# Performance work log

Hardware: AMD Instinct MI355X
Metric: run time of the kernel (lower is better)

The kernel has to match this reference:

```python
import jax, jax.numpy as jnp
import numpy as np

NJ, ND, NQ, NC, NAV = 4, 32, 32, 64, 2
N = 131072

def silu(x):
    return x * jax.nn.sigmoid(x)

def conv1d(x, w, b, stride=1):
    # x: [n, Cin, L], w: [Cout, Cin, K] (torch OIH layout)
    y = jax.lax.conv_general_dilated(x, w, (stride,), 'VALID',
                                     dimension_numbers=('NCH', 'OIH', 'NCH'))
    return y + b[None, :, None]

def dijet_cat(x, d):
    # x: [n, nd, 12], d: [n, nd, 6] -> interleave pairs of x with d -> [n, nd, 18]
    n, nd, _ = x.shape
    return jnp.concatenate([x.reshape(n, nd, 6, 2), d[..., None]], axis=3).reshape(n, nd, 18)

def quad_cat(x, q):
    # x: [n, nq, 6], q: [n, nq, 3] -> [n, nq, 9]
    n, nq, _ = x.shape
    return jnp.concatenate([x.reshape(n, nq, 3, 2), q[..., None]], axis=3).reshape(n, nq, 9)

def rotate(p, R):
    return p.at[:, 2, :].set(((p[:, 2, :] + 1.0 + R) % 2.0) - 1.0)

def flip_phi(p):
    return p.at[:, 2, :].multiply(-1.0)

def flip_eta(p):
    return p.at[:, 1, :].multiply(-1.0)

def inv_part(p, da, qa, W_td, b_td, W_db, b_db, W_dr1, b_dr1, W_dr2, b_dr2,
             W_tq, b_tq, W_qb, b_qb, W_qr1, b_qr1, W_qr2, b_qr2):
    p = conv1d(p, W_td, b_td)                 # [n, nd, 12]
    d = conv1d(p, W_db, b_db, stride=2)       # [n, nd-2, 6]
    d = jnp.concatenate([d, da], axis=1)      # [n, nd, 6]
    d0 = d
    d = silu(d)
    d = conv1d(dijet_cat(p, d), W_dr1, b_dr1, stride=3) + d0
    d = silu(d)
    d = conv1d(dijet_cat(p, d), W_dr2, b_dr2, stride=3) + d0
    d = silu(d)
    d = conv1d(d, W_tq, b_tq)                 # [n, nq, 6]
    q = conv1d(d, W_qb, b_qb, stride=2)       # [n, nq-2, 3]
    q = jnp.concatenate([q, qa], axis=1)      # [n, nq, 3]
    q0 = q
    q = silu(q)
    q = conv1d(quad_cat(d, q), W_qr1, b_qr1, stride=3) + q0
    q = silu(q)
    q = conv1d(quad_cat(d, q), W_qr2, b_qr2, stride=3) + q0
    return silu(q)                            # [n, nq, 3]

def setup_inputs() -> dict:
    key = jax.random.key(0)
    ks = jax.random.split(key, 24)
    s = 0.1
    inp = {
        'x': jax.random.normal(ks[0], (N, NJ, 12), jnp.float32),
        'p': jax.random.normal(ks[1], (N, NJ, 12), jnp.float32),
        'da': jax.random.normal(ks[2], (N, 12), jnp.float32),
        'qa': jax.random.normal(ks[3], (N, 6), jnp.float32),
        'va': jax.random.normal(ks[4], (N, NAV), jnp.float32),
        'W_td': jax.random.normal(ks[5], (ND, NJ, 1), jnp.float32) * s,
        'b_td': jax.random.normal(ks[6], (ND,), jnp.float32) * s,
        'W_db': jax.random.normal(ks[7], (ND - 2, ND, 2), jnp.float32) * s,
        'b_db': jax.random.normal(ks[8], (ND - 2,), jnp.float32) * s,
        'W_dr1': jax.random.normal(ks[9], (ND, ND, 3), jnp.float32) * s,
        'b_dr1': jax.random.normal(ks[10], (ND,), jnp.float32) * s,
        'W_dr2': jax.random.normal(ks[11], (ND, ND, 3), jnp.float32) * s,
        'b_dr2': jax.random.normal(ks[12], (ND,), jnp.float32) * s,
        'W_tq': jax.random.normal(ks[13], (NQ, ND, 1), jnp.float32) * s,
        'b_tq': jax.random.normal(ks[14], (NQ,), jnp.float32) * s,
        'W_qb': jax.random.normal(ks[15], (NQ - 2, NQ, 2), jnp.float32) * s,
        'b_qb': jax.random.normal(ks[16], (NQ - 2,), jnp.float32) * s,
        'W_qr1': jax.random.normal(ks[17], (NQ, NQ, 3), jnp.float32) * s,
        'b_qr1': jax.random.normal(ks[18], (NQ,), jnp.float32) * s,
        'W_qr2': jax.random.normal(ks[19], (NQ, NQ, 3), jnp.float32) * s,
        'b_qr2': jax.random.normal(ks[20], (NQ,), jnp.float32) * s,
        'W_tv': jax.random.normal(ks[21], (NC, NQ + NAV, 1), jnp.float32) * s,
        'b_tv': jax.random.normal(ks[22], (NC,), jnp.float32) * s,
        'W_v1': jax.random.normal(jax.random.fold_in(key, 101), (NC, NC, 1), jnp.float32) * s,
        'b_v1': jax.random.normal(jax.random.fold_in(key, 102), (NC,), jnp.float32) * s,
        'W_v2': jax.random.normal(jax.random.fold_in(key, 103), (NC, NC, 1), jnp.float32) * s,
        'b_v2': jax.random.normal(jax.random.fold_in(key, 104), (NC,), jnp.float32) * s,
        'W_vs': jax.random.normal(jax.random.fold_in(key, 105), (1, NC, 3), jnp.float32) * s,
        'b_vs': jax.random.normal(jax.random.fold_in(key, 106), (1,), jnp.float32) * s,
    }
    return inp

def reference(x, p, da, qa, va,
              W_td, b_td, W_db, b_db, W_dr1, b_dr1, W_dr2, b_dr2,
              W_tq, b_tq, W_qb, b_qb, W_qr1, b_qr1, W_qr2, b_qr2,
              W_tv, b_tv, W_v1, b_v1, W_v2, b_v2, W_vs, b_vs):
    n = p.shape[0]
    da2 = da.reshape(n, 2, 6)
    qa2 = qa.reshape(n, 2, 3)
    va3 = jnp.broadcast_to(va[:, :NAV, None], (n, NAV, 3))
    params = (W_td, b_td, W_db, b_db, W_dr1, b_dr1, W_dr2, b_dr2,
              W_tq, b_tq, W_qb, b_qb, W_qr1, b_qr1, W_qr2, b_qr2)
    # eval mode: nR=1, R=[0], randomR=0; 4-fold phi/eta flip symmetrization
    p0 = rotate(p, 0.0)
    p1 = flip_phi(p0)
    p2 = flip_eta(p1)
    p3 = flip_eta(p0)
    q = (inv_part(p0, da2, qa2, *params) + inv_part(p1, da2, qa2, *params)
         + inv_part(p2, da2, qa2, *params) + inv_part(p3, da2, qa2, *params)) / 4.0
    v = jnp.concatenate([q, va3], axis=1)     # [n, nq+nAv, 3]
    v = conv1d(v, W_tv, b_tv)                 # [n, nc, 3]
    v0 = v
    v = silu(v)
    v = conv1d(v, W_v1, b_v1) + v0
    v = silu(v)
    v = conv1d(v, W_v2, b_v2) + v0
    v = silu(v)
    v = conv1d(v, W_vs, b_vs)                 # [n, 1, 1]
    return v.reshape(n, -1)
```

## Files before the change

### kernel.cpp

```cpp
#include <hip/hip_runtime.h>


typedef _Float16 f16x8 __attribute__((ext_vector_type(8)));
typedef float f32x4 __attribute__((ext_vector_type(4)));
typedef __fp16 fp16x2 __attribute__((ext_vector_type(2)));

#define TILES 50
#define WS_BIAS    12800
#define NBIAS      416
#define QSUM_DW    13216

__device__ __forceinline__ float silu_f(float x){
    return x * __builtin_amdgcn_rcpf(1.0f + __expf(-x));
}
__device__ __forceinline__ f32x4 silu4(f32x4 v){
    f32x4 r; r.x=silu_f(v.x); r.y=silu_f(v.y); r.z=silu_f(v.z); r.w=silu_f(v.w);
    return r;
}
__device__ __forceinline__ unsigned pk(float a, float b){
    fp16x2 h = __builtin_amdgcn_cvt_pkrtz(a, b);
    return __builtin_bit_cast(unsigned, h);
}


__device__ float l1_Ad0(const float* Wdb, const float* Wtd, int c, int k){
    int h = k>>2, jr = k&3; float a = 0.f;
    for (int i=0;i<32;++i) a += Wdb[64*c+2*i+h]*Wtd[4*i+jr];
    return a;
}
__device__ float l1_AB(const float* Wdb,const float* bdb,const float* btd,int c){
    float b = bdb[c];
    for (int i=0;i<32;++i) b += (Wdb[64*c+2*i]+Wdb[64*c+2*i+1])*btd[i];
    return b;
}
__device__ float l1_M(const float* Wdr,const float* Wtd,int c,int k){
    int h=k>>2, jr=k&3; float a=0.f;
    for(int i=0;i<32;++i) a += Wdr[96*c+3*i+h]*Wtd[4*i+jr];
    return a;
}
__device__ float l1_MB(const float* Wdr,const float* bdr,const float* btd,int c){
    float b = bdr[c];
    for(int i=0;i<32;++i) b += (Wdr[96*c+3*i]+Wdr[96*c+3*i+1])*btd[i];
    return b;
}
__device__ float qn_Q(const float* Wqb, const float* Wtq, int c, int kg){
    int z=kg>>5, kk=kg&31; float a=0.f;
    for(int i=0;i<32;++i) a += Wqb[64*c+2*i+z]*Wtq[32*i+kk];
    return a;
}
__device__ float qn_N(const float* Wqr, const float* Wtq, int c, int kg){
    int z=kg>>5, kk=kg&31; float a=0.f;
    for(int i=0;i<32;++i) a += Wqr[96*c+3*i+z]*Wtq[32*i+kk];
    return a;
}

__global__ void precompute(
    const float* __restrict__ Wtd, const float* __restrict__ btd,
    const float* __restrict__ Wdb, const float* __restrict__ bdb,
    const float* __restrict__ Wdr1, const float* __restrict__ bdr1,
    const float* __restrict__ Wdr2, const float* __restrict__ bdr2,
    const float* __restrict__ Wtq, const float* __restrict__ btq,
    const float* __restrict__ Wqb, const float* __restrict__ bqb,
    const float* __restrict__ Wqr1, const float* __restrict__ bqr1,
    const float* __restrict__ Wqr2, const float* __restrict__ bqr2,
    const float* __restrict__ Wtv, const float* __restrict__ btv,
    const float* __restrict__ Wv1, const float* __restrict__ bv1,
    const float* __restrict__ Wv2, const float* __restrict__ bv2,
    const float* __restrict__ Wvs,
    float* __restrict__ wsf)
{
    const int tid = blockIdx.x*blockDim.x + threadIdx.x;
    const int stride = gridDim.x*blockDim.x;

    for (int it = tid; it < TILES*64; it += stride) {
        const int tile = it >> 6, lane = it & 63;
        const int m = lane & 15, g = lane >> 4;
        float v[8];
        #pragma unroll
        for (int j = 0; j < 8; ++j) {
            const int k = 8*g + j;
            float val = 0.f;
            if (tile < 6) {
                const int r = 16*tile + m;
                if (r < 32) {
                    if (r < 30) {
                        if (k < 8)      val = l1_Ad0(Wdb, Wtd, r, k);
                        else if (k==8)  val = l1_AB(Wdb, bdb, btd, r);
                    } else if (r == 30) val = (k==9)  ? 1.f : 0.f;
                    else                val = (k==10) ? 1.f : 0.f;
                } else {
                    const float* Wdr = (r<64)? Wdr1 : Wdr2;
                    const float* bdr = (r<64)? bdr1 : bdr2;
                    const int c = (r<64)? r-32 : r-64;
                    if (k < 8) {
                        val = l1_M(Wdr, Wtd, c, k);
                        if (c < 30) val += l1_Ad0(Wdb, Wtd, c, k);
                    } else if (k == 8) {
                        val = l1_MB(Wdr, bdr, btd, c);
                        if (c < 30) val += l1_AB(Wdb, bdb, btd, c);
                    } else if (k == 9)  val = (c==30)? 1.f : 0.f;
                    else if (k == 10)   val = (c==31)? 1.f : 0.f;
                }
            } else if (tile < 8)  { val = Wdr1[96*(16*(tile-6)+m) + 3*k + 2]; }
            else if (tile < 10)   { val = Wdr2[96*(16*(tile-8)+m) + 3*k + 2]; }
            else if (tile < 22) {
                const int tt = tile-10, r = 16*(tt>>1)+m, kg = 32*(tt&1)+k;
                if (r < 32) { if (r < 30) val = qn_Q(Wqb, Wtq, r, kg); }
                else {
                    const float* Wqr = (r<64)? Wqr1 : Wqr2;
                    const int c = (r<64)? r-32 : r-64;
                    val = qn_N(Wqr, Wtq, c, kg);
                    if (c < 30) val += qn_Q(Wqb, Wtq, c, kg);
                }
            }
            else if (tile < 24)  { val = Wqr1[96*(16*(tile-22)+m) + 3*k + 2]; }
            else if (tile < 26)  { val = Wqr2[96*(16*(tile-24)+m) + 3*k + 2]; }
            else if (tile < 34) {
                const int tt = tile-26, r = 16*(tt>>1)+m;
                if ((tt&1)==0) val = 0.25f*Wtv[34*r + k];
                else {
                    if (k==0) val = btv[r];
                    else if (k==1) val = Wtv[34*r+32];
                    else if (k==2) val = Wtv[34*r+33];
                }
            }
            else if (tile < 42) { const int tt=tile-34; val = Wv1[64*(16*(tt>>1)+m) + 32*(tt&1) + k]; }
            else                { const int tt=tile-42; val = Wv2[64*(16*(tt>>1)+m) + 32*(tt&1) + k]; }
            v[j] = val;
        }
        unsigned* wd = (unsigned*)wsf;
        const int base = tile*256 + lane*4;
        wd[base+0] = pk(v[0],v[1]);
        wd[base+1] = pk(v[2],v[3]);
        wd[base+2] = pk(v[4],v[5]);
        wd[base+3] = pk(v[6],v[7]);
    }

    for (int r = tid; r < NBIAS; r += stride) {
        float val = 0.f;
        if (r < 96) {
            if (r < 30) {
                float b = bqb[r];
                for (int i=0;i<32;++i) b += (Wqb[64*r+2*i]+Wqb[64*r+2*i+1])*btq[i];
                val = b;
            } else if (r >= 32) {
                const float* Wqr = (r<64)? Wqr1 : Wqr2;
                const float* bqr = (r<64)? bqr1 : bqr2;
                const int c = (r<64)? r-32 : r-64;
                float b = bqr[c];
                for (int i=0;i<32;++i) b += (Wqr[96*c+3*i]+Wqr[96*c+3*i+1])*btq[i];
                if (c < 30) {
                    float qb = bqb[c];
                    for (int i=0;i<32;++i) qb += (Wqb[64*c+2*i]+Wqb[64*c+2*i+1])*btq[i];
                    b += qb;
                }
                val = b;
            }
        }
        else if (r < 160) val = bv1[r-96];
        else if (r < 224) val = bv2[r-160];
        else { const int idx = r-224, lq = idx>>6, row = idx&63; val = Wvs[3*row + lq]; }
        wsf[WS_BIAS + r] = val;
    }
}


__global__ __launch_bounds__(256, 2) void resnet_part1(
    const float* __restrict__ P,  const float* __restrict__ DA,
    const float* __restrict__ QA, const float* __restrict__ wsf,
    unsigned* __restrict__ qsum, int n_total)
{
    __shared__ uint4 lw[26*64];
    __shared__ alignas(16) float fbA[96];

    {
        const uint4* src = (const uint4*)wsf;
        for (int i = threadIdx.x; i < 26*64; i += blockDim.x) lw[i] = src[i];
        uint4* fb4 = (uint4*)fbA;
        for (int i = threadIdx.x; i < 24; i += blockDim.x) fb4[i] = src[3200 + i];
    }
    __syncthreads();

    const int l  = threadIdx.x & 63;
    const int wv = threadIdx.x >> 6;
    const int c  = l & 15, g = l >> 4;
    const int s  = blockIdx.x*64 + wv*16 + c;
    const int sl = (s < n_total) ? s : (n_total-1);
    const bool g0 = (g==0), g1 = (g==1);

    const uint4* lwl = lw + l;
    #define LDA(T) __builtin_bit_cast(f16x8, lwl[(T)*64])
    #define MFMA(A,B,C) __builtin_amdgcn_mfma_f32_16x16x32_f16((A), __builtin_bit_cast(f16x8,(B)), (C), 0, 0, 0)

    const int srcA = ((l>>4)&1)*32 + (l&15);
    const int srcB = srcA + 16;
    const bool hiT = (l >= 32);
    #define REPACK(RES, T0, T1) {                                              \
        unsigned plo0 = pk((T0).x,(T0).y), phi0 = pk((T0).z,(T0).w);           \
        unsigned plo1 = pk((T1).x,(T1).y), phi1 = pk((T1).z,(T1).w);           \
        unsigned a0 = (unsigned)__shfl((int)plo0, srcA, 64);                   \
        unsigned a1 = (unsigned)__shfl((int)plo1, srcA, 64);                   \
        unsigned b0 = (unsigned)__shfl((int)phi0, srcA, 64);                   \
        unsigned b1 = (unsigned)__shfl((int)phi1, srcA, 64);                   \
        unsigned c0 = (unsigned)__shfl((int)plo0, srcB, 64);                   \
        unsigned c1 = (unsigned)__shfl((int)plo1, srcB, 64);                   \
        unsigned d0 = (unsigned)__shfl((int)phi0, srcB, 64);                   \
        unsigned d1 = (unsigned)__shfl((int)phi1, srcB, 64);                   \
        (RES).x = hiT?a1:a0; (RES).y = hiT?b1:b0;                              \
        (RES).z = hiT?c1:c0; (RES).w = hiT?d1:d0; }

    const unsigned me = g0 ? 0x80000000u : 0u;
    const unsigned mp = g0 ? 0x00008000u : 0u;

    const f32x4 z4 = {0.f,0.f,0.f,0.f};

    #pragma unroll 1
    for (int lq = 0; lq < 3; ++lq) {
        uint4 xb[2];
        #pragma unroll
        for (int t = 0; t < 2; ++t) {
            const int pos = 4*lq + 2*t;
            float f0 = P[48*sl + pos],        f1 = P[48*sl + 12 + pos];
            float y0 = P[48*sl + 24 + pos] + 1.0f; y0 -= 2.0f*floorf(y0*0.5f);
            float f2 = y0 - 1.0f,             f3 = P[48*sl + 36 + pos];
            float f4 = P[48*sl + pos + 1],    f5 = P[48*sl + 12 + pos + 1];
            float y1 = P[48*sl + 24 + pos + 1] + 1.0f; y1 -= 2.0f*floorf(y1*0.5f);
            float f6 = y1 - 1.0f,             f7 = P[48*sl + 36 + pos + 1];
            float da0 = DA[12*sl + 2*lq + t];
            float da1 = DA[12*sl + 6 + 2*lq + t];
            uint4 xv; xv.x=0; xv.y=0; xv.z=0; xv.w=0;
            if (g0)      { xv.x = pk(f0,f1); xv.y = pk(f2,f3); xv.z = pk(f4,f5); xv.w = pk(f6,f7); }
            else if (g1) { xv.x = pk(1.0f, da0); xv.y = pk(da1, 0.0f); }
            xb[t] = xv;
        }
        const float qa30m = (g==3) ? QA[6*sl + lq]     : 0.0f;
        const float qa31m = (g==3) ? QA[6*sl + 3 + lq] : 0.0f;

        f32x4 qav0 = z4, qav1 = z4;

        #pragma unroll 1
        for (int var = 0; var < 4; ++var) {
            const unsigned fe = (var>=2)? me : 0u;
            const unsigned fp = (var==1||var==2)? mp : 0u;

            uint4 Bs[2];
            #pragma unroll
            for (int t = 0; t < 2; ++t) {
                uint4 Bxi;
                Bxi.x = xb[t].x ^ fe; Bxi.y = xb[t].y ^ fp;
                Bxi.z = xb[t].z ^ fe; Bxi.w = xb[t].w ^ fp;

                f32x4 a0 = MFMA(LDA(0), Bxi, z4);
                f32x4 a1 = MFMA(LDA(1), Bxi, z4);
                f32x4 a2 = MFMA(LDA(2), Bxi, z4);
                f32x4 a3 = MFMA(LDA(3), Bxi, z4);
                f32x4 a4 = MFMA(LDA(4), Bxi, z4);
                f32x4 a5 = MFMA(LDA(5), Bxi, z4);

                uint4 Bt;
                { f32x4 s0=silu4(a0), s1=silu4(a1); REPACK(Bt, s0, s1); }
                a2 = MFMA(LDA(6), Bt, a2);
                a3 = MFMA(LDA(7), Bt, a3);
                { f32x4 s0=silu4(a2), s1=silu4(a3); REPACK(Bt, s0, s1); }
                a4 = MFMA(LDA(8), Bt, a4);
                a5 = MFMA(LDA(9), Bt, a5);
                { f32x4 s0=silu4(a4), s1=silu4(a5); REPACK(Bs[t], s0, s1); }
            }

            f32x4 q[6];
            #pragma unroll
            for (int mt=0; mt<6; ++mt) {
                f32x4 acc = MFMA(LDA(10+2*mt), Bs[0], *(const f32x4*)&fbA[16*mt + 4*g]);
                q[mt] = MFMA(LDA(10+2*mt+1), Bs[1], acc);
            }
            q[1].z += qa30m; q[1].w += qa31m;
            q[3].z += qa30m; q[3].w += qa31m;
            q[5].z += qa30m; q[5].w += qa31m;

            uint4 Bq;
            { f32x4 s0=silu4(q[0]), s1=silu4(q[1]); REPACK(Bq, s0, s1); }
            q[2] = MFMA(LDA(22), Bq, q[2]);
            q[3] = MFMA(LDA(23), Bq, q[3]);
            { f32x4 s0=silu4(q[2]), s1=silu4(q[3]); REPACK(Bq, s0, s1); }
            q[4] = MFMA(LDA(24), Bq, q[4]);
            q[5] = MFMA(LDA(25), Bq, q[5]);
            qav0 += silu4(q[4]);
            qav1 += silu4(q[5]);
        }

        if (s < n_total) {
            const int rec = (lq*n_total + sl)*16;
            uint2 w0; w0.x = pk(qav0.x, qav0.y); w0.y = pk(qav0.z, qav0.w);
            uint2 w1; w1.x = pk(qav1.x, qav1.y); w1.y = pk(qav1.z, qav1.w);
            *(uint2*)&qsum[rec + 2*g]     = w0;
            *(uint2*)&qsum[rec + 8 + 2*g] = w1;
        }
    }
}


__global__ __launch_bounds__(256, 3) void resnet_part2(
    const float* __restrict__ VA, const float* __restrict__ wsf,
    const unsigned* __restrict__ qsum, const float* __restrict__ bvs,
    float* __restrict__ out, int n_total)
{
    __shared__ uint4 lw2[24*64];
    __shared__ alignas(16) float fbB[320];

    {
        const uint4* src = (const uint4*)wsf;
        for (int i = threadIdx.x; i < 24*64; i += blockDim.x) lw2[i] = src[26*64 + i];
        uint4* fb4 = (uint4*)fbB;
        for (int i = threadIdx.x; i < 80; i += blockDim.x) fb4[i] = src[3224 + i];
    }
    __syncthreads();

    const int l  = threadIdx.x & 63;
    const int wv = threadIdx.x >> 6;
    const int c  = l & 15, g = l >> 4;
    const int s  = blockIdx.x*64 + wv*16 + c;
    const int sl = (s < n_total) ? s : (n_total-1);
    const bool g0 = (g==0);

    const uint4* lwl = lw2 + l;
    #define LDB(T) __builtin_bit_cast(f16x8, lwl[((T)-26)*64])

    uint4 Bva; Bva.x=0; Bva.y=0; Bva.z=0; Bva.w=0;
    if (g0) {
        const float va0 = VA[2*sl], va1 = VA[2*sl+1];
        Bva.x = pk(1.0f, va0); Bva.y = pk(va1, 0.0f);
    }

    const int srcA = ((l>>4)&1)*32 + (l&15);
    const int srcB = srcA + 16;
    const bool hiT = (l >= 32);

    const f32x4 z4 = {0.f,0.f,0.f,0.f};
    float out_acc = 0.0f;

    #pragma unroll 1
    for (int lq = 0; lq < 3; ++lq) {
        const uint4 BQ = *(const uint4*)&qsum[(lq*n_total + sl)*16 + 4*g];

        f32x4 uacc[4], w[4];
        #pragma unroll
        for (int mt=0; mt<4; ++mt) {
            f32x4 acc = MFMA(LDB(26+2*mt), BQ, z4);
            uacc[mt] = MFMA(LDB(27+2*mt), Bva, acc);
        }
        uint4 B0, B1;
        { f32x4 t0=silu4(uacc[0]), t1=silu4(uacc[1]); REPACK(B0, t0, t1); }
        { f32x4 t0=silu4(uacc[2]), t1=silu4(uacc[3]); REPACK(B1, t0, t1); }
        #pragma unroll
        for (int mt=0; mt<4; ++mt) {
            f32x4 acc = MFMA(LDB(34+2*mt), B0, uacc[mt]);
            acc = MFMA(LDB(35+2*mt), B1, acc);
            w[mt] = acc + *(const f32x4*)&fbB[16*mt + 4*g];
        }
        { f32x4 t0=silu4(w[0]), t1=silu4(w[1]); REPACK(B0, t0, t1); }
        { f32x4 t0=silu4(w[2]), t1=silu4(w[3]); REPACK(B1, t0, t1); }
        #pragma unroll
        for (int mt=0; mt<4; ++mt) {
            f32x4 acc = MFMA(LDB(42+2*mt), B0, uacc[mt]);
            acc = MFMA(LDB(43+2*mt), B1, acc);
            w[mt] = acc + *(const f32x4*)&fbB[64 + 16*mt + 4*g];
        }
        #pragma unroll
        for (int mt=0; mt<4; ++mt) {
            const f32x4 wvs = *(const f32x4*)&fbB[128 + 64*lq + 16*mt + 4*g];
            out_acc += wvs.x*silu_f(w[mt].x) + wvs.y*silu_f(w[mt].y)
                     + wvs.z*silu_f(w[mt].z) + wvs.w*silu_f(w[mt].w);
        }
    }

    out_acc += __shfl_xor(out_acc, 16, 64);
    out_acc += __shfl_xor(out_acc, 32, 64);
    if (g == 0 && s < n_total) out[s] = out_acc + bvs[0];
}

extern "C" void kernel_launch(void* const* d_in, const int* in_sizes, int n_in,
                              void* d_out, int out_size, void* d_ws, size_t ws_size,
                              hipStream_t stream)
{
    (void)n_in; (void)ws_size; (void)out_size;
    const float* P   = (const float*)d_in[1];
    const float* DA  = (const float*)d_in[2];
    const float* QA  = (const float*)d_in[3];
    const float* VA  = (const float*)d_in[4];
    const float* Wtd = (const float*)d_in[5];   const float* btd = (const float*)d_in[6];
    const float* Wdb = (const float*)d_in[7];   const float* bdb = (const float*)d_in[8];
    const float* Wdr1= (const float*)d_in[9];   const float* bdr1= (const float*)d_in[10];
    const float* Wdr2= (const float*)d_in[11];  const float* bdr2= (const float*)d_in[12];
    const float* Wtq = (const float*)d_in[13];  const float* btq = (const float*)d_in[14];
    const float* Wqb = (const float*)d_in[15];  const float* bqb = (const float*)d_in[16];
    const float* Wqr1= (const float*)d_in[17];  const float* bqr1= (const float*)d_in[18];
    const float* Wqr2= (const float*)d_in[19];  const float* bqr2= (const float*)d_in[20];
    const float* Wtv = (const float*)d_in[21];  const float* btv = (const float*)d_in[22];
    const float* Wv1 = (const float*)d_in[23];  const float* bv1 = (const float*)d_in[24];
    const float* Wv2 = (const float*)d_in[25];  const float* bv2 = (const float*)d_in[26];
    const float* Wvs = (const float*)d_in[27];  const float* bvs = (const float*)d_in[28];
    float* out = (float*)d_out;

    const int n_total = in_sizes[1] / 48;
    float* wsf = (float*)d_ws;
    unsigned* qsum = (unsigned*)(wsf + QSUM_DW);

    precompute<<<dim3(64), dim3(256), 0, stream>>>(
        Wtd, btd, Wdb, bdb, Wdr1, bdr1, Wdr2, bdr2,
        Wtq, btq, Wqb, bqb, Wqr1, bqr1, Wqr2, bqr2,
        Wtv, btv, Wv1, bv1, Wv2, bv2, Wvs, wsf);

    const int grid = (n_total + 63) / 64;
    resnet_part1<<<dim3(grid), dim3(256), 0, stream>>>(
        P, DA, QA, wsf, qsum, n_total);
    resnet_part2<<<dim3(grid), dim3(256), 0, stream>>>(
        VA, wsf, qsum, bvs, out, n_total);
}
```

Measured before the change: 236.1 us.

## Permute weight K-columns so MFMA outputs feed next MFMA without shuffles

Weight tiles for consumer layers are now built with a permuted input-channel index (CIN) that matches the register layout the previous MFMA's accumulator leaves in each lane. The activation can then be packed directly into the B operand with plain fp16 packing, replacing the eight cross-lane shuffles per REPACK. The qsum record store is also simplified to one 16-byte write per lane in the matching order. This moves layout work into the one-time weight preprocessing and relies on the permutation exactly matching the MFMA accumulator layout.

```diff
diff --git a/kernel.cpp b/kernel.cpp
--- a/kernel.cpp
+++ b/kernel.cpp
@@ -10,6 +10,8 @@
 #define NBIAS      416
 #define QSUM_DW    13216
 
+#define CIN(k) (16*(((k)>>2)&1) + 4*((k)>>3) + ((k)&3))
+
 __device__ __forceinline__ float silu_f(float x){
     return x * __builtin_amdgcn_rcpf(1.0f + __expf(-x));
 }
@@ -21,6 +23,9 @@
     fp16x2 h = __builtin_amdgcn_cvt_pkrtz(a, b);
     return __builtin_bit_cast(unsigned, h);
 }
+#define PACKB(RES, T0, T1) {                                                   \
+    (RES).x = pk((T0).x,(T0).y); (RES).y = pk((T0).z,(T0).w);                  \
+    (RES).z = pk((T1).x,(T1).y); (RES).w = pk((T1).z,(T1).w); }
 
 
 __device__ float l1_Ad0(const float* Wdb, const float* Wtd, int c, int k){
@@ -101,10 +106,10 @@
                     } else if (k == 9)  val = (c==30)? 1.f : 0.f;
                     else if (k == 10)   val = (c==31)? 1.f : 0.f;
                 }
-            } else if (tile < 8)  { val = Wdr1[96*(16*(tile-6)+m) + 3*k + 2]; }
-            else if (tile < 10)   { val = Wdr2[96*(16*(tile-8)+m) + 3*k + 2]; }
+            } else if (tile < 8)  { val = Wdr1[96*(16*(tile-6)+m) + 3*CIN(k) + 2]; }
+            else if (tile < 10)   { val = Wdr2[96*(16*(tile-8)+m) + 3*CIN(k) + 2]; }
             else if (tile < 22) {
-                const int tt = tile-10, r = 16*(tt>>1)+m, kg = 32*(tt&1)+k;
+                const int tt = tile-10, r = 16*(tt>>1)+m, kg = 32*(tt&1)+CIN(k);
                 if (r < 32) { if (r < 30) val = qn_Q(Wqb, Wtq, r, kg); }
                 else {
                     const float* Wqr = (r<64)? Wqr1 : Wqr2;
@@ -113,19 +118,19 @@
                     if (c < 30) val += qn_Q(Wqb, Wtq, c, kg);
                 }
             }
-            else if (tile < 24)  { val = Wqr1[96*(16*(tile-22)+m) + 3*k + 2]; }
-            else if (tile < 26)  { val = Wqr2[96*(16*(tile-24)+m) + 3*k + 2]; }
+            else if (tile < 24)  { val = Wqr1[96*(16*(tile-22)+m) + 3*CIN(k) + 2]; }
+            else if (tile < 26)  { val = Wqr2[96*(16*(tile-24)+m) + 3*CIN(k) + 2]; }
             else if (tile < 34) {
                 const int tt = tile-26, r = 16*(tt>>1)+m;
-                if ((tt&1)==0) val = 0.25f*Wtv[34*r + k];
+                if ((tt&1)==0) val = 0.25f*Wtv[34*r + CIN(k)];
                 else {
                     if (k==0) val = btv[r];
                     else if (k==1) val = Wtv[34*r+32];
                     else if (k==2) val = Wtv[34*r+33];
                 }
             }
-            else if (tile < 42) { const int tt=tile-34; val = Wv1[64*(16*(tt>>1)+m) + 32*(tt&1) + k]; }
-            else                { const int tt=tile-42; val = Wv2[64*(16*(tt>>1)+m) + 32*(tt&1) + k]; }
+            else if (tile < 42) { const int tt=tile-34; val = Wv1[64*(16*(tt>>1)+m) + 32*(tt&1) + CIN(k)]; }
+            else                { const int tt=tile-42; val = Wv2[64*(16*(tt>>1)+m) + 32*(tt&1) + CIN(k)]; }
             v[j] = val;
         }
         unsigned* wd = (unsigned*)wsf;
@@ -192,23 +197,6 @@
     #define LDA(T) __builtin_bit_cast(f16x8, lwl[(T)*64])
     #define MFMA(A,B,C) __builtin_amdgcn_mfma_f32_16x16x32_f16((A), __builtin_bit_cast(f16x8,(B)), (C), 0, 0, 0)
 
-    const int srcA = ((l>>4)&1)*32 + (l&15);
-    const int srcB = srcA + 16;
-    const bool hiT = (l >= 32);
-    #define REPACK(RES, T0, T1) {                                              \
-        unsigned plo0 = pk((T0).x,(T0).y), phi0 = pk((T0).z,(T0).w);           \
-        unsigned plo1 = pk((T1).x,(T1).y), phi1 = pk((T1).z,(T1).w);           \
-        unsigned a0 = (unsigned)__shfl((int)plo0, srcA, 64);                   \
-        unsigned a1 = (unsigned)__shfl((int)plo1, srcA, 64);                   \
-        unsigned b0 = (unsigned)__shfl((int)phi0, srcA, 64);                   \
-        unsigned b1 = (unsigned)__shfl((int)phi1, srcA, 64);                   \
-        unsigned c0 = (unsigned)__shfl((int)plo0, srcB, 64);                   \
-        unsigned c1 = (unsigned)__shfl((int)plo1, srcB, 64);                   \
-        unsigned d0 = (unsigned)__shfl((int)phi0, srcB, 64);                   \
-        unsigned d1 = (unsigned)__shfl((int)phi1, srcB, 64);                   \
-        (RES).x = hiT?a1:a0; (RES).y = hiT?b1:b0;                              \
-        (RES).z = hiT?c1:c0; (RES).w = hiT?d1:d0; }
-
     const unsigned me = g0 ? 0x80000000u : 0u;
     const unsigned mp = g0 ? 0x00008000u : 0u;
 
@@ -258,13 +246,13 @@
                 f32x4 a5 = MFMA(LDA(5), Bxi, z4);
 
                 uint4 Bt;
-                { f32x4 s0=silu4(a0), s1=silu4(a1); REPACK(Bt, s0, s1); }
+                { f32x4 s0=silu4(a0), s1=silu4(a1); PACKB(Bt, s0, s1); }
                 a2 = MFMA(LDA(6), Bt, a2);
                 a3 = MFMA(LDA(7), Bt, a3);
-                { f32x4 s0=silu4(a2), s1=silu4(a3); REPACK(Bt, s0, s1); }
+                { f32x4 s0=silu4(a2), s1=silu4(a3); PACKB(Bt, s0, s1); }
                 a4 = MFMA(LDA(8), Bt, a4);
                 a5 = MFMA(LDA(9), Bt, a5);
-                { f32x4 s0=silu4(a4), s1=silu4(a5); REPACK(Bs[t], s0, s1); }
+                { f32x4 s0=silu4(a4), s1=silu4(a5); PACKB(Bs[t], s0, s1); }
             }
 
             f32x4 q[6];
@@ -278,10 +266,10 @@
             q[5].z += qa30m; q[5].w += qa31m;
 
             uint4 Bq;
-            { f32x4 s0=silu4(q[0]), s1=silu4(q[1]); REPACK(Bq, s0, s1); }
+            { f32x4 s0=silu4(q[0]), s1=silu4(q[1]); PACKB(Bq, s0, s1); }
             q[2] = MFMA(LDA(22), Bq, q[2]);
             q[3] = MFMA(LDA(23), Bq, q[3]);
-            { f32x4 s0=silu4(q[2]), s1=silu4(q[3]); REPACK(Bq, s0, s1); }
+            { f32x4 s0=silu4(q[2]), s1=silu4(q[3]); PACKB(Bq, s0, s1); }
             q[4] = MFMA(LDA(24), Bq, q[4]);
             q[5] = MFMA(LDA(25), Bq, q[5]);
             qav0 += silu4(q[4]);
@@ -290,10 +278,8 @@
 
         if (s < n_total) {
             const int rec = (lq*n_total + sl)*16;
-            uint2 w0; w0.x = pk(qav0.x, qav0.y); w0.y = pk(qav0.z, qav0.w);
-            uint2 w1; w1.x = pk(qav1.x, qav1.y); w1.y = pk(qav1.z, qav1.w);
-            *(uint2*)&qsum[rec + 2*g]     = w0;
-            *(uint2*)&qsum[rec + 8 + 2*g] = w1;
+            uint4 w0; PACKB(w0, qav0, qav1);
+            *(uint4*)&qsum[rec + 4*g] = w0;
         }
     }
 }
@@ -331,10 +317,6 @@
         Bva.x = pk(1.0f, va0); Bva.y = pk(va1, 0.0f);
     }
 
-    const int srcA = ((l>>4)&1)*32 + (l&15);
-    const int srcB = srcA + 16;
-    const bool hiT = (l >= 32);
-
     const f32x4 z4 = {0.f,0.f,0.f,0.f};
     float out_acc = 0.0f;
 
@@ -349,16 +331,16 @@
             uacc[mt] = MFMA(LDB(27+2*mt), Bva, acc);
         }
         uint4 B0, B1;
-        { f32x4 t0=silu4(uacc[0]), t1=silu4(uacc[1]); REPACK(B0, t0, t1); }
-        { f32x4 t0=silu4(uacc[2]), t1=silu4(uacc[3]); REPACK(B1, t0, t1); }
+        { f32x4 t0=silu4(uacc[0]), t1=silu4(uacc[1]); PACKB(B0, t0, t1); }
+        { f32x4 t0=silu4(uacc[2]), t1=silu4(uacc[3]); PACKB(B1, t0, t1); }
         #pragma unroll
         for (int mt=0; mt<4; ++mt) {
             f32x4 acc = MFMA(LDB(34+2*mt), B0, uacc[mt]);
             acc = MFMA(LDB(35+2*mt), B1, acc);
             w[mt] = acc + *(const f32x4*)&fbB[16*mt + 4*g];
         }
-        { f32x4 t0=silu4(w[0]), t1=silu4(w[1]); REPACK(B0, t0, t1); }
-        { f32x4 t0=silu4(w[2]), t1=silu4(w[3]); REPACK(B1, t0, t1); }
+        { f32x4 t0=silu4(w[0]), t1=silu4(w[1]); PACKB(B0, t0, t1); }
+        { f32x4 t0=silu4(w[2]), t1=silu4(w[3]); PACKB(B1, t0, t1); }
         #pragma unroll
         for (int mt=0; mt<4; ++mt) {
             f32x4 acc = MFMA(LDB(42+2*mt), B0, uacc[mt]);
```

Result: faster. 214.1 us (-9.4%).
